# Kernel tuning notes

Measured on AMD Instinct MI355X. Metric: run time of the kernel, lower is better.

Reference implementation:

```python
import jax, jax.numpy as jnp
import numpy as np

DT = 0.01
NLAG = 50           # int(maxlag / dt), maxlag = 0.5 s
NMA = 20
NC = 8192
NT = 4096


def _xcorr(data1, data2):
    # torch F.conv1d(data1.view(1, nc, nt), data2.view(nc, 1, nt),
    #                padding=NLAG+1, groups=nc)
    # == per-channel sliding cross-correlation.
    lhs = data1[None]            # (1, NC, NT)
    rhs = data2[:, None, :]      # (NC, 1, NT) -- one tiny filter per group
    out = jax.lax.conv_general_dilated(
        lhs, rhs,
        window_strides=(1,),
        padding=[(NLAG + 1, NLAG + 1)],
        dimension_numbers=("NCH", "OIH", "NCH"),
        feature_group_count=NC,
    )
    return out                   # (1, NC, L), L = 2*NLAG + 3 when nt1 == nt2


def _moving_average(x, nma=NMA):
    # Faithful to CCModel.moving_average: AvgPool1d(nma, stride=1, pad=nma//2)
    # applied after permute(0,2,1), i.e. the pooling runs over the CHANNEL
    # axis, with zero padding included in the mean (count_include_pad=True),
    # then sliced back to nc channels.
    nb, nc, L = x.shape
    pad = nma // 2
    xp = jnp.pad(x, ((0, 0), (pad, pad), (0, 0)))
    cs = jnp.concatenate(
        [jnp.zeros((nb, 1, L), x.dtype), jnp.cumsum(xp, axis=1)], axis=1)
    win = (cs[:, nma:, :] - cs[:, :-nma, :]) / nma   # sliding sum / nma
    return win[:, :nc, :]


def _pick_maxabs(R, dt):
    # pick_Rkt_maxabs: per-channel max-|cc| pick.
    L = R.shape[-1]
    nlag_c = (L - 1) // 2        # zero-lag index
    imax = jnp.argmax(jnp.abs(R), axis=-1)                              # (nb, nc)
    vmain = jnp.take_along_axis(R, imax[..., None], axis=-1)[..., 0]    # signed peak
    vpos = jnp.max(R, axis=-1)
    vneg = jnp.min(R, axis=-1)
    vside = jnp.where(vmain >= 0, vneg, vpos)        # opposite-sign extremum
    tmax = (imax - nlag_c).astype(R.dtype) * dt
    return vmain, vside, tmax


def setup_inputs() -> dict:
    key = jax.random.key(0)
    k1, k2, k3, k4 = jax.random.split(key, 4)
    data1 = jax.random.normal(k1, (NC, NT), dtype=jnp.float32)
    data2 = jax.random.normal(k2, (NC, NT), dtype=jnp.float32)
    event1 = jax.random.randint(k3, (1,), 0, 1000, dtype=jnp.int32)
    event2 = jax.random.randint(k4, (1,), 0, 1000, dtype=jnp.int32)
    return {"data1": data1, "data2": data2, "event1": event1, "event2": event2}


def reference(data1, data2, event1, event2):
    xcor = _xcorr(data1, data2)              # (1, NC, 2*NLAG+3)
    xcor = _moving_average(xcor, NMA)        # in-place overwrite in torch
    vmax, vmin, tmax = _pick_maxabs(xcor, DT)
    return xcor, vmax, vmin, tmax
```

## Files before the change

kernel.cpp:

```cpp
#include <hip/hip_runtime.h>

#define NC 8192
#define NT 4096
#define NLAGS 103
#define WS_STRIDE 104
#define LPW 28
#define PADL 51
#define D1LOG 4208
#define PHYS(x) ((x) + (((x) >> 4) << 2))
#define D1P 5260
#define D2P 5120
#define SMEMF (D1P + D2P)
#define XBASE (NC*NLAGS)

__global__ __launch_bounds__(256, 3)
void xcorr_kernel(const float* __restrict__ g1, const float* __restrict__ g2,
                  float* __restrict__ ws) {
    __shared__ __align__(16) float smem[SMEMF];
    float* d1s = smem;
    float* d2s = smem + D1P;
    const int c   = blockIdx.x;
    const int tid = threadIdx.x;
    const float4* r14 = (const float4*)(g1 + (size_t)c * NT);
    const float4* r24 = (const float4*)(g2 + (size_t)c * NT);

    #pragma unroll
    for (int i = 0; i < 4; ++i) {
        float4 v = r14[tid + 256*i];
        int x = PADL + 4*(tid + 256*i);
        d1s[PHYS(x)]   = v.x;
        d1s[PHYS(x+1)] = v.y;
        d1s[PHYS(x+2)] = v.z;
        d1s[PHYS(x+3)] = v.w;
        float4 u = r24[tid + 256*i];
        int y = 4*(tid + 256*i);
        *(float4*)&d2s[PHYS(y)] = u;
    }
    if (tid < PADL) d1s[PHYS(tid)] = 0.f;
    if (tid < 61)   d1s[PHYS(PADL + NT + tid)] = 0.f;
    __syncthreads();

    const int wv   = tid >> 6;
    const int lane = tid & 63;
    const int l0   = wv * LPW;

    float acc[LPW];
    #pragma unroll
    for (int l = 0; l < LPW; ++l) acc[l] = 0.f;

    #pragma unroll 1
    for (int it = 0; it < 4; ++it) {
        const int k0 = it*1024 + lane*16;
        float b[16];
        #pragma unroll
        for (int t = 0; t < 4; ++t) {
            int y = k0 + 4*t;
            float4 v = *(const float4*)&d2s[PHYS(y)];
            b[4*t]=v.x; b[4*t+1]=v.y; b[4*t+2]=v.z; b[4*t+3]=v.w;
        }
        float w[LPW + 16];
        #pragma unroll
        for (int t = 0; t < 11; ++t) {
            int x = k0 + l0 + 4*t;
            float4 v = *(const float4*)&d1s[PHYS(x)];
            w[4*t]=v.x; w[4*t+1]=v.y; w[4*t+2]=v.z; w[4*t+3]=v.w;
        }
        #pragma unroll
        for (int j = 0; j < 16; ++j)
            #pragma unroll
            for (int l = 0; l < LPW; ++l)
                acc[l] = fmaf(w[l+j], b[j], acc[l]);
    }

    __syncthreads();
    float* red = smem + wv * (64*29);
    #pragma unroll
    for (int l = 0; l < LPW; ++l) red[lane*29 + l] = acc[l];
    float sum = 0.f;
    const int lcol = lane & 31;
    const int rb   = lane & 32;
    #pragma unroll
    for (int r = 0; r < 32; ++r) sum += red[(rb + r)*29 + lcol];
    sum += __shfl_down(sum, 32);
    const int L = l0 + lcol;
    if (lane < LPW && L < NLAGS)
        ws[(size_t)c * WS_STRIDE + L] = sum;
}

#define TS 112
__global__ __launch_bounds__(256, 4)
void ma_pick_kernel(const float* __restrict__ ws, float* __restrict__ out) {
    __shared__ float tile[52*TS];
    __shared__ float matile[32*TS];
    const int tid = threadIdx.x;
    const int c0  = blockIdx.x * 32;

    for (int i = tid; i < 52*TS; i += 256) {
        int r   = i / TS;
        int col = i - r*TS;
        int g   = c0 - 10 + r;
        float v = 0.f;
        if (g >= 0 && g < NC && col < NLAGS) v = ws[(size_t)g*WS_STRIDE + col];
        tile[i] = v;
    }
    __syncthreads();

    {
        const int l = tid & 127;
        const int h = tid >> 7;
        if (l < NLAGS) {
            const int cc0 = h * 16;
            float s = 0.f;
            #pragma unroll
            for (int r = 0; r < 20; ++r) s += tile[(cc0 + r)*TS + l];
            #pragma unroll 1
            for (int cc = cc0; cc < cc0 + 16; ++cc) {
                float ma = s / 20.0f;
                matile[cc*TS + l] = ma;
                out[(size_t)(c0 + cc)*NLAGS + l] = ma;
                s += tile[(cc + 20)*TS + l] - tile[cc*TS + l];
            }
        }
    }
    __syncthreads();

    const int wv = tid >> 6, lane = tid & 63;
    #pragma unroll 1
    for (int s8 = 0; s8 < 8; ++s8) {
        const int cc = wv*8 + s8;
        float v1 = matile[cc*TS + lane];
        float a1 = fabsf(v1);
        int   i1 = lane;
        float vmx = v1, vmn = v1;
        if (lane < NLAGS - 64) {
            float v2 = matile[cc*TS + 64 + lane];
            float a2 = fabsf(v2);
            vmx = fmaxf(vmx, v2); vmn = fminf(vmn, v2);
            if (a2 > a1) { a1 = a2; i1 = 64 + lane; v1 = v2; }
        }
        #pragma unroll
        for (int d = 32; d >= 1; d >>= 1) {
            float oa  = __shfl_xor(a1, d);
            int   oi  = __shfl_xor(i1, d);
            float ov  = __shfl_xor(v1, d);
            float omx = __shfl_xor(vmx, d);
            float omn = __shfl_xor(vmn, d);
            vmx = fmaxf(vmx, omx);
            vmn = fminf(vmn, omn);
            if (oa > a1 || (oa == a1 && oi < i1)) { a1 = oa; i1 = oi; v1 = ov; }
        }
        if (lane == 0) {
            const int ch = c0 + cc;
            out[XBASE + ch]        = v1;
            out[XBASE + NC + ch]   = (v1 >= 0.f) ? vmn : vmx;
            out[XBASE + 2*NC + ch] = (float)(i1 - 51) * 0.01f;
        }
    }
}

extern "C" void kernel_launch(void* const* d_in, const int* in_sizes, int n_in,
                              void* d_out, int out_size, void* d_ws, size_t ws_size,
                              hipStream_t stream) {
    const float* g1 = (const float*)d_in[0];
    const float* g2 = (const float*)d_in[1];
    float* out = (float*)d_out;
    float* ws  = (float*)d_ws;

    hipLaunchKernelGGL(xcorr_kernel, dim3(NC), dim3(256), 0, stream, g1, g2, ws);
    hipLaunchKernelGGL(ma_pick_kernel, dim3(NC/32), dim3(256), 0, stream, ws, out);
}
```

Before: 318.4 us.

## Drop padded LDS layout, interleave lanes over 4-tap chunks, raise occupancy

```diff
diff --git a/kernel.cpp b/kernel.cpp
--- a/kernel.cpp
+++ b/kernel.cpp
@@ -5,20 +5,17 @@
 #define NLAGS 103
 #define WS_STRIDE 104
 #define LPW 28
-#define PADL 51
-#define D1LOG 4208
-#define PHYS(x) ((x) + (((x) >> 4) << 2))
-#define D1P 5260
-#define D2P 5120
-#define SMEMF (D1P + D2P)
+#define D1OFF 52
+#define D1SZ 4272
+#define SMEMF (D1SZ + NT)
 #define XBASE (NC*NLAGS)
 
-__global__ __launch_bounds__(256, 3)
+__global__ __launch_bounds__(256, 4)
 void xcorr_kernel(const float* __restrict__ g1, const float* __restrict__ g2,
                   float* __restrict__ ws) {
     __shared__ __align__(16) float smem[SMEMF];
     float* d1s = smem;
-    float* d2s = smem + D1P;
+    float* d2s = smem + D1SZ;
     const int c   = blockIdx.x;
     const int tid = threadIdx.x;
     const float4* r14 = (const float4*)(g1 + (size_t)c * NT);
@@ -26,50 +23,38 @@
 
     #pragma unroll
     for (int i = 0; i < 4; ++i) {
-        float4 v = r14[tid + 256*i];
-        int x = PADL + 4*(tid + 256*i);
-        d1s[PHYS(x)]   = v.x;
-        d1s[PHYS(x+1)] = v.y;
-        d1s[PHYS(x+2)] = v.z;
-        d1s[PHYS(x+3)] = v.w;
-        float4 u = r24[tid + 256*i];
-        int y = 4*(tid + 256*i);
-        *(float4*)&d2s[PHYS(y)] = u;
+        ((float4*)(d1s + D1OFF))[tid + 256*i] = r14[tid + 256*i];
+        ((float4*)d2s)[tid + 256*i]           = r24[tid + 256*i];
     }
-    if (tid < PADL) d1s[PHYS(tid)] = 0.f;
-    if (tid < 61)   d1s[PHYS(PADL + NT + tid)] = 0.f;
+    if (tid < D1OFF) d1s[tid] = 0.f;
+    if (tid < 124)   d1s[D1OFF + NT + tid] = 0.f;
     __syncthreads();
 
     const int wv   = tid >> 6;
     const int lane = tid & 63;
-    const int l0   = wv * LPW;
+    const int l0   = LPW*wv - 1;
+    const int wb0  = 4*lane + LPW*wv;
 
     float acc[LPW];
     #pragma unroll
     for (int l = 0; l < LPW; ++l) acc[l] = 0.f;
 
     #pragma unroll 1
-    for (int it = 0; it < 4; ++it) {
-        const int k0 = it*1024 + lane*16;
-        float b[16];
+    for (int p = 0; p < 16; ++p) {
+        const int k0 = p << 8;
+        float w[32];
         #pragma unroll
-        for (int t = 0; t < 4; ++t) {
-            int y = k0 + 4*t;
-            float4 v = *(const float4*)&d2s[PHYS(y)];
-            b[4*t]=v.x; b[4*t+1]=v.y; b[4*t+2]=v.z; b[4*t+3]=v.w;
-        }
-        float w[LPW + 16];
-        #pragma unroll
-        for (int t = 0; t < 11; ++t) {
-            int x = k0 + l0 + 4*t;
-            float4 v = *(const float4*)&d1s[PHYS(x)];
+        for (int t = 0; t < 8; ++t) {
+            float4 v = *(const float4*)&d1s[k0 + wb0 + 4*t];
             w[4*t]=v.x; w[4*t+1]=v.y; w[4*t+2]=v.z; w[4*t+3]=v.w;
         }
+        float4 bv = *(const float4*)&d2s[k0 + 4*lane];
+        const float b[4] = {bv.x, bv.y, bv.z, bv.w};
         #pragma unroll
-        for (int j = 0; j < 16; ++j)
+        for (int j = 0; j < 4; ++j)
             #pragma unroll
             for (int l = 0; l < LPW; ++l)
-                acc[l] = fmaf(w[l+j], b[j], acc[l]);
+                acc[l] = fmaf(w[j + l], b[j], acc[l]);
     }
 
     __syncthreads();
@@ -83,7 +68,7 @@
     for (int r = 0; r < 32; ++r) sum += red[(rb + r)*29 + lcol];
     sum += __shfl_down(sum, 32);
     const int L = l0 + lcol;
-    if (lane < LPW && L < NLAGS)
+    if (lane < LPW && L >= 0 && L < NLAGS)
         ws[(size_t)c * WS_STRIDE + L] = sum;
 }
 
```

After: 444.0 us. 1.39x slower.
